# Kernel tuning notes

Hardware: AMD Instinct MI355X
Metric: run time of the kernel (lower is better)

## Reference

```python
import jax, jax.numpy as jnp
import numpy as np

EPS = 1e-7
N = 100000
E = 1600000
IN_DIM = 128
OUT_DIM = 128


def _norm(t):
    # clamped L2 norm over last dim, keepdims
    return jnp.clip(jnp.linalg.norm(t, axis=-1, keepdims=True), EPS, None)


def log_map_zero(x, c):
    sqrt_c = jnp.sqrt(c)
    xn = _norm(x)
    y = jnp.clip(sqrt_c * xn, None, 1.0 - 1e-5)
    return jnp.arctanh(y) * x / (sqrt_c * xn)


def exp_map_zero(v, c):
    sqrt_c = jnp.sqrt(c)
    vn = _norm(v)
    return jnp.tanh(sqrt_c * vn) * v / (sqrt_c * vn)


def setup_inputs() -> dict:
    key = jax.random.key(0)
    k1, k2, k3, k4 = jax.random.split(key, 4)
    x = 0.1 * jax.random.normal(k1, (N, IN_DIM), dtype=jnp.float32)  # inside ball
    edge_index = jax.random.randint(k2, (2, E), 0, N, dtype=jnp.int64)
    c = jnp.ones((), dtype=jnp.float32)
    # Xavier-uniform weight (out_dim, in_dim)
    limit = float(np.sqrt(6.0 / (IN_DIM + OUT_DIM)))
    weight = jax.random.uniform(k3, (OUT_DIM, IN_DIM), minval=-limit, maxval=limit, dtype=jnp.float32)
    bias = jnp.zeros((OUT_DIM,), dtype=jnp.float32)
    return {"x": x, "edge_index": edge_index, "c": c, "num_nodes": N,
            "weight": weight, "bias": bias}


def reference(x, edge_index, c, num_nodes, weight, bias):
    # 1. log-map all node features to tangent space at origin
    v = log_map_zero(x, c)  # (N, in_dim)
    src, dst = edge_index[0], edge_index[1]
    # 2. mean aggregation over neighbours (incl. self) via segment_sum
    agg = jax.ops.segment_sum(v[src], dst, num_segments=num_nodes) + v
    count = jax.ops.segment_sum(jnp.ones((src.shape[0],), dtype=v.dtype), dst,
                                num_segments=num_nodes) + 1.0
    v_agg = agg / jnp.clip(count, 1.0, None)[:, None]
    # 3. back to hyperbolic space, then hyperbolic linear
    x_hyp = exp_map_zero(v_agg, c)
    v2 = log_map_zero(x_hyp, c)
    out = v2 @ weight.T + bias
    return exp_map_zero(out, c)
```

## Files before the change

kernel.cpp:

```cpp
#include <hip/hip_runtime.h>
#include <math.h>

#define EPSF 1e-7f
#define YMAXF 0.99999f
#define WPITCH 136

#define NBUCK 256
#define PB_CHUNK 2048

typedef short bf16x8 __attribute__((ext_vector_type(8)));
typedef short bf16x4 __attribute__((ext_vector_type(4)));
typedef float f32x4  __attribute__((ext_vector_type(4)));

__device__ __forceinline__ float grp32_sum(float v) {
    v += __shfl_xor(v, 1);
    v += __shfl_xor(v, 2);
    v += __shfl_xor(v, 4);
    v += __shfl_xor(v, 8);
    v += __shfl_xor(v, 16);
    return v;
}

__device__ __forceinline__ short f2bf(float f) {
    unsigned u = __float_as_uint(f);
    unsigned r = (u + 0x7FFFu + ((u >> 16) & 1u)) >> 16;
    return (short)r;
}

__device__ __forceinline__ float bf2f(short u) {
    return __uint_as_float(((unsigned)(unsigned short)u) << 16);
}

__global__ void logmap_kernel(const float* __restrict__ x,
                              const float* __restrict__ c_ptr,
                              short* __restrict__ v_bf,
                              int N) {
    int gid = blockIdx.x * blockDim.x + threadIdx.x;
    int row = gid >> 5;
    if (row >= N) return;
    int lane = gid & 31;
    const float4 xv = ((const float4*)x)[(size_t)row * 32 + lane];
    float ss = xv.x * xv.x + xv.y * xv.y + xv.z * xv.z + xv.w * xv.w;
    ss = grp32_sum(ss);
    float sc = sqrtf(c_ptr[0]);
    float xn = fmaxf(sqrtf(ss), EPSF);
    float y = fminf(sc * xn, YMAXF);
    float s = atanhf(y) / (sc * xn);
    bf16x4 pk;
    pk[0] = f2bf(s * xv.x); pk[1] = f2bf(s * xv.y);
    pk[2] = f2bf(s * xv.z); pk[3] = f2bf(s * xv.w);
    *(bf16x4*)&v_bf[(size_t)row * 128 + lane * 4] = pk;
}

__global__ __launch_bounds__(256)
void bucket_count_kernel(const int* __restrict__ eidx_dst,
                         int* __restrict__ bucketCount, int E) {
    __shared__ int h[NBUCK];
    int tid = threadIdx.x;
    h[tid] = 0;
    __syncthreads();
    int per = (E + gridDim.x - 1) / gridDim.x;
    int start = blockIdx.x * per;
    int end = min(start + per, E);
    for (int i = start + tid; i < end; i += 256)
        atomicAdd(&h[eidx_dst[i] >> 9], 1);
    __syncthreads();
    if (h[tid]) atomicAdd(&bucketCount[tid], h[tid]);
}

__global__ __launch_bounds__(256)
void bucket_scan_kernel(const int* __restrict__ bucketCount,
                        int* __restrict__ bucket_base,
                        int* __restrict__ cursor) {
    __shared__ int part[256];
    int tid = threadIdx.x;
    int val = bucketCount[tid];
    part[tid] = val;
    __syncthreads();
    for (int off = 1; off < 256; off <<= 1) {
        int t = (tid >= off) ? part[tid - off] : 0;
        __syncthreads();
        part[tid] += t;
        __syncthreads();
    }
    int excl = part[tid] - val;
    bucket_base[tid] = excl;
    cursor[tid] = excl;
}

__global__ __launch_bounds__(256)
void bucket_scatter_kernel(const int* __restrict__ eidx,
                           int* __restrict__ cursor,
                           int* __restrict__ bucketed, int E) {
    __shared__ int hist[NBUCK];
    __shared__ int lstart[NBUCK];
    __shared__ int gbase[NBUCK];
    __shared__ int part[256];
    __shared__ int stage[PB_CHUNK];
    __shared__ unsigned char stageB[PB_CHUNK];

    int tid = threadIdx.x;
    int start = blockIdx.x * PB_CHUNK;
    int cnt = min(PB_CHUNK, E - start);
    hist[tid] = 0;
    __syncthreads();

    const int J = PB_CHUNK / 256;
    int myP[J], myB[J], myR[J];
    #pragma unroll
    for (int j = 0; j < J; ++j) {
        int idx = j * 256 + tid;
        myR[j] = -1;
        if (idx < cnt) {
            int e = start + idx;
            int d = eidx[E + e];
            int s = eidx[e];
            int b = d >> 9;
            myB[j] = b;
            myP[j] = ((d & 511) << 17) | s;
            myR[j] = atomicAdd(&hist[b], 1);
        }
    }
    __syncthreads();
    part[tid] = hist[tid];
    __syncthreads();
    for (int off = 1; off < 256; off <<= 1) {
        int t = (tid >= off) ? part[tid - off] : 0;
        __syncthreads();
        part[tid] += t;
        __syncthreads();
    }
    lstart[tid] = part[tid] - hist[tid];
    if (hist[tid]) gbase[tid] = atomicAdd(&cursor[tid], hist[tid]);
    __syncthreads();
    #pragma unroll
    for (int j = 0; j < J; ++j) {
        if (myR[j] >= 0) {
            int pos = lstart[myB[j]] + myR[j];
            stage[pos] = myP[j];
            stageB[pos] = (unsigned char)myB[j];
        }
    }
    __syncthreads();
    for (int i = tid; i < cnt; i += 256) {
        int b = stageB[i];
        bucketed[gbase[b] + (i - lstart[b])] = stage[i];
    }
}

__global__ __launch_bounds__(256)
void csr_kernel(const int* __restrict__ bucketed,
                const int* __restrict__ bucket_base,
                const int* __restrict__ cursor_post,
                int* __restrict__ offsets, int* __restrict__ deg,
                int* __restrict__ sorted_src, int N) {
    __shared__ int hist[512];
    __shared__ int pre[512];
    __shared__ int cur[512];
    __shared__ int part[256];
    int b = blockIdx.x;
    int tid = threadIdx.x;
    int start = bucket_base[b];
    int end = cursor_post[b];
    hist[tid] = 0;
    hist[tid + 256] = 0;
    __syncthreads();
    for (int i = start + tid; i < end; i += 256)
        atomicAdd(&hist[bucketed[i] >> 17], 1);
    __syncthreads();
    int a0 = hist[2 * tid], a1 = hist[2 * tid + 1];
    part[tid] = a0 + a1;
    __syncthreads();
    for (int off = 1; off < 256; off <<= 1) {
        int t = (tid >= off) ? part[tid - off] : 0;
        __syncthreads();
        part[tid] += t;
        __syncthreads();
    }
    int base2 = part[tid] - (a0 + a1);
    pre[2 * tid] = base2;
    pre[2 * tid + 1] = base2 + a0;
    cur[2 * tid] = base2;
    cur[2 * tid + 1] = base2 + a0;
    __syncthreads();
    int node0 = b << 9;
    for (int i = tid; i < 512; i += 256) {
        int node = node0 + i;
        if (node < N) { offsets[node] = start + pre[i]; deg[node] = hist[i]; }
    }
    for (int i = start + tid; i < end; i += 256) {
        int p = bucketed[i];
        int ld = p >> 17;
        int src = p & 0x1FFFF;
        int r = atomicAdd(&cur[ld], 1);
        sorted_src[start + r] = src;
    }
}

__global__ __launch_bounds__(256)
void gather_epilogue_kernel(const short* __restrict__ v_bf,
                            const int* __restrict__ sorted_src,
                            const int* __restrict__ offsets,
                            const int* __restrict__ deg,
                            const float* __restrict__ W,
                            const float* __restrict__ bias,
                            const float* __restrict__ c_ptr,
                            float* __restrict__ out,
                            int N, int tiles_per_block) {
    __shared__ short Wl[128 * WPITCH];
    __shared__ short v2l[16 * WPITCH];
    __shared__ float bias_s[128];
    __shared__ float outss[16][4];
    __shared__ float gscale[16];

    int tid = threadIdx.x;
    for (int i = tid; i < 4096; i += 256) {
        float4 w4 = ((const float4*)W)[i];
        int o = i >> 5;
        int k = (i & 31) * 4;
        bf16x4 w;
        w[0] = f2bf(w4.x); w[1] = f2bf(w4.y); w[2] = f2bf(w4.z); w[3] = f2bf(w4.w);
        *(bf16x4*)&Wl[o * WPITCH + k] = w;
    }
    if (tid < 128) bias_s[tid] = bias[tid];
    float sc = sqrtf(c_ptr[0]);
    __syncthreads();

    int wave = tid >> 6;
    int lane = tid & 63;
    int quad = lane >> 4;
    int l16  = lane & 15;
    int g  = tid >> 4;
    int gl = tid & 15;
    int n0 = wave * 32;
    float b0 = bias_s[n0 + l16];
    float b1 = bias_s[n0 + 16 + l16];

    for (int t = 0; t < tiles_per_block; ++t) {
        int row0 = (blockIdx.x * tiles_per_block + t) * 16;
        if (row0 >= N) break;
        int row = row0 + g;
        bool valid = (row < N);

        float acc[8];
        #pragma unroll
        for (int i = 0; i < 8; ++i) acc[i] = 0.0f;
        int start = 0, d = 0;
        if (valid) {
            start = offsets[row];
            d = deg[row];
            bf16x8 r0 = *(const bf16x8*)&v_bf[(size_t)row * 128 + gl * 8];
            #pragma unroll
            for (int i = 0; i < 8; ++i) acc[i] = bf2f(r0[i]);
        }
        for (int j = 0; j < d; j += 16) {
            int idx = j + gl;
            int batch = (idx < d) ? sorted_src[start + idx] : 0;
            int m = min(16, d - j);
            for (int jj = 0; jj < m; ++jj) {
                int src = __shfl(batch, (lane & 48) | jj);
                bf16x8 r = *(const bf16x8*)&v_bf[(size_t)src * 128 + gl * 8];
                #pragma unroll
                for (int i = 0; i < 8; ++i) acc[i] += bf2f(r[i]);
            }
        }
        float inv = 1.0f / (float)(d + 1);
        #pragma unroll
        for (int i = 0; i < 8; ++i) acc[i] *= inv;

        float ss = 0.0f;
        #pragma unroll
        for (int i = 0; i < 8; ++i) ss += acc[i] * acc[i];
        ss += __shfl_xor(ss, 1);
        ss += __shfl_xor(ss, 2);
        ss += __shfl_xor(ss, 4);
        ss += __shfl_xor(ss, 8);

        float vn  = sqrtf(ss);
        float vnc = fmaxf(vn, EPSF);
        float th  = tanhf(sc * vnc);
        float tt  = th / (sc * vnc);
        float hn  = fmaxf(th / sc, EPSF);
        float y2  = fminf(sc * hn, YMAXF);
        float s2  = atanhf(y2) / (sc * hn);
        float scale = s2 * tt;

        bf16x8 pk;
        #pragma unroll
        for (int i = 0; i < 8; ++i) pk[i] = f2bf(acc[i] * scale);
        *(bf16x8*)&v2l[g * WPITCH + gl * 8] = pk;
        __syncthreads();

        f32x4 acc0 = {b0, b0, b0, b0};
        f32x4 acc1 = {b1, b1, b1, b1};
        #pragma unroll
        for (int k0 = 0; k0 < 128; k0 += 32) {
            bf16x8 af  = *(const bf16x8*)&v2l[l16 * WPITCH + k0 + quad * 8];
            bf16x8 bf0 = *(const bf16x8*)&Wl[(n0 + l16) * WPITCH + k0 + quad * 8];
            bf16x8 bf1 = *(const bf16x8*)&Wl[(n0 + 16 + l16) * WPITCH + k0 + quad * 8];
            acc0 = __builtin_amdgcn_mfma_f32_16x16x32_bf16(af, bf0, acc0, 0, 0, 0);
            acc1 = __builtin_amdgcn_mfma_f32_16x16x32_bf16(af, bf1, acc1, 0, 0, 0);
        }

        float pss[4];
        #pragma unroll
        for (int r = 0; r < 4; ++r) {
            float vsum = acc0[r]*acc0[r] + acc1[r]*acc1[r];
            vsum += __shfl_xor(vsum, 1);
            vsum += __shfl_xor(vsum, 2);
            vsum += __shfl_xor(vsum, 4);
            vsum += __shfl_xor(vsum, 8);
            pss[r] = vsum;
        }
        if (l16 == 0) {
            #pragma unroll
            for (int r = 0; r < 4; ++r) outss[quad * 4 + r][wave] = pss[r];
        }
        __syncthreads();
        if (tid < 16) {
            float on  = sqrtf(outss[tid][0] + outss[tid][1] + outss[tid][2] + outss[tid][3]);
            float onc = fmaxf(on, EPSF);
            gscale[tid] = tanhf(sc * onc) / (sc * onc);
        }
        __syncthreads();
        #pragma unroll
        for (int r = 0; r < 4; ++r) {
            int orow = quad * 4 + r;
            if (row0 + orow < N) {
                float gsc = gscale[orow];
                size_t base = (size_t)(row0 + orow) * 128;
                out[base + n0 + l16]      = gsc * acc0[r];
                out[base + n0 + 16 + l16] = gsc * acc1[r];
            }
        }
        __syncthreads();
    }
}

extern "C" void kernel_launch(void* const* d_in, const int* in_sizes, int n_in,
                              void* d_out, int out_size, void* d_ws, size_t ws_size,
                              hipStream_t stream) {
    const float* x     = (const float*)d_in[0];
    const int*   eidx  = (const int*)d_in[1];
    const float* c_ptr = (const float*)d_in[2];
    const float* W     = (const float*)d_in[4];
    const float* bias  = (const float*)d_in[5];
    float* out = (float*)d_out;

    int N = in_sizes[0] / 128;
    int E = in_sizes[1] / 2;

    short* v_bf        = (short*)d_ws;
    int*   deg         = (int*)(v_bf + (size_t)N * 128);
    int*   offsets     = deg + N;
    int*   bucketCount = offsets + N;
    int*   bucket_base = bucketCount + NBUCK;
    int*   cursor      = bucket_base + NBUCK;
    int*   bucketed    = cursor + NBUCK;
    int*   sorted_src  = bucketed + E;

    hipMemsetAsync(bucketCount, 0, NBUCK * sizeof(int), stream);

    {
        long long threads = (long long)N * 32;
        int blocks = (int)((threads + 255) / 256);
        hipLaunchKernelGGL(logmap_kernel, dim3(blocks), dim3(256), 0, stream,
                           x, c_ptr, v_bf, N);
    }
    hipLaunchKernelGGL(bucket_count_kernel, dim3(256), dim3(256), 0, stream,
                       eidx + E, bucketCount, E);
    hipLaunchKernelGGL(bucket_scan_kernel, dim3(1), dim3(256), 0, stream,
                       bucketCount, bucket_base, cursor);
    {
        int blocks = (E + PB_CHUNK - 1) / PB_CHUNK;
        hipLaunchKernelGGL(bucket_scatter_kernel, dim3(blocks), dim3(256), 0, stream,
                           eidx, cursor, bucketed, E);
    }
    {
        int blocks = (N + 511) / 512;
        hipLaunchKernelGGL(csr_kernel, dim3(blocks), dim3(256), 0, stream,
                           bucketed, bucket_base, cursor, offsets, deg, sorted_src, N);
    }
    {
        const int TPB = 5;
        int numTiles = (N + 15) / 16;
        int blocks = (numTiles + TPB - 1) / TPB;
        hipLaunchKernelGGL(gather_epilogue_kernel, dim3(blocks), dim3(256), 0, stream,
                           v_bf, sorted_src, offsets, deg, W, bias, c_ptr, out, N, TPB);
    }
}
```

Before: 312.2 us.

## Batch neighbor loads and restructure gather epilogue into 64-row blocks with per-wave GEMM

```diff
diff --git a/kernel.cpp b/kernel.cpp
--- a/kernel.cpp
+++ b/kernel.cpp
@@ -11,6 +11,7 @@
 typedef short bf16x8 __attribute__((ext_vector_type(8)));
 typedef short bf16x4 __attribute__((ext_vector_type(4)));
 typedef float f32x4  __attribute__((ext_vector_type(4)));
+typedef int   i32x4  __attribute__((ext_vector_type(4)));
 
 __device__ __forceinline__ float grp32_sum(float v) {
     v += __shfl_xor(v, 1);
@@ -29,6 +30,13 @@
 
 __device__ __forceinline__ float bf2f(short u) {
     return __uint_as_float(((unsigned)(unsigned short)u) << 16);
+}
+
+__device__ __forceinline__ float bf_lo(int w) {
+    return __uint_as_float(((unsigned)w) << 16);
+}
+__device__ __forceinline__ float bf_hi(int w) {
+    return __uint_as_float(((unsigned)w) & 0xffff0000u);
 }
 
 __global__ void logmap_kernel(const float* __restrict__ x,
@@ -197,7 +205,7 @@
     }
 }
 
-__global__ __launch_bounds__(256)
+__global__ __launch_bounds__(256, 3)
 void gather_epilogue_kernel(const short* __restrict__ v_bf,
                             const int* __restrict__ sorted_src,
                             const int* __restrict__ offsets,
@@ -206,12 +214,9 @@
                             const float* __restrict__ bias,
                             const float* __restrict__ c_ptr,
                             float* __restrict__ out,
-                            int N, int tiles_per_block) {
+                            int N) {
     __shared__ short Wl[128 * WPITCH];
-    __shared__ short v2l[16 * WPITCH];
-    __shared__ float bias_s[128];
-    __shared__ float outss[16][4];
-    __shared__ float gscale[16];
+    __shared__ short v2l[64 * WPITCH];
 
     int tid = threadIdx.x;
     for (int i = tid; i < 4096; i += 256) {
@@ -222,9 +227,6 @@
         w[0] = f2bf(w4.x); w[1] = f2bf(w4.y); w[2] = f2bf(w4.z); w[3] = f2bf(w4.w);
         *(bf16x4*)&Wl[o * WPITCH + k] = w;
     }
-    if (tid < 128) bias_s[tid] = bias[tid];
-    float sc = sqrtf(c_ptr[0]);
-    __syncthreads();
 
     int wave = tid >> 6;
     int lane = tid & 63;
@@ -232,16 +234,17 @@
     int l16  = lane & 15;
     int g  = tid >> 4;
     int gl = tid & 15;
-    int n0 = wave * 32;
-    float b0 = bias_s[n0 + l16];
-    float b1 = bias_s[n0 + 16 + l16];
-
-    for (int t = 0; t < tiles_per_block; ++t) {
-        int row0 = (blockIdx.x * tiles_per_block + t) * 16;
-        if (row0 >= N) break;
-        int row = row0 + g;
+    float sc = sqrtf(c_ptr[0]);
+
+    float bsv[8];
+    #pragma unroll
+    for (int c = 0; c < 8; ++c) bsv[c] = bias[c * 16 + l16];
+
+    int row_base = blockIdx.x * 64;
+
+    for (int t = 0; t < 4; ++t) {
+        int row = row_base + t * 16 + g;
         bool valid = (row < N);
-
         float acc[8];
         #pragma unroll
         for (int i = 0; i < 8; ++i) acc[i] = 0.0f;
@@ -250,18 +253,35 @@
             start = offsets[row];
             d = deg[row];
             bf16x8 r0 = *(const bf16x8*)&v_bf[(size_t)row * 128 + gl * 8];
+            i32x4 w0 = *(const i32x4*)&r0;
             #pragma unroll
-            for (int i = 0; i < 8; ++i) acc[i] = bf2f(r0[i]);
+            for (int k2 = 0; k2 < 4; ++k2) {
+                acc[2 * k2]     = bf_lo(w0[k2]);
+                acc[2 * k2 + 1] = bf_hi(w0[k2]);
+            }
         }
         for (int j = 0; j < d; j += 16) {
+            int m = d - j;
             int idx = j + gl;
-            int batch = (idx < d) ? sorted_src[start + idx] : 0;
-            int m = min(16, d - j);
-            for (int jj = 0; jj < m; ++jj) {
-                int src = __shfl(batch, (lane & 48) | jj);
-                bf16x8 r = *(const bf16x8*)&v_bf[(size_t)src * 128 + gl * 8];
-                #pragma unroll
-                for (int i = 0; i < 8; ++i) acc[i] += bf2f(r[i]);
+            int batch = sorted_src[start + min(idx, d - 1)];
+            bf16x8 r[16];
+            #pragma unroll
+            for (int jj = 0; jj < 16; ++jj) {
+                if (jj < m) {
+                    int src = __shfl(batch, (lane & 48) | jj);
+                    r[jj] = *(const bf16x8*)&v_bf[(size_t)src * 128 + gl * 8];
+                }
+            }
+            #pragma unroll
+            for (int jj = 0; jj < 16; ++jj) {
+                if (jj < m) {
+                    i32x4 wv = *(const i32x4*)&r[jj];
+                    #pragma unroll
+                    for (int k2 = 0; k2 < 4; ++k2) {
+                        acc[2 * k2]     += bf_lo(wv[k2]);
+                        acc[2 * k2 + 1] += bf_hi(wv[k2]);
+                    }
+                }
             }
         }
         float inv = 1.0f / (float)(d + 1);
@@ -288,52 +308,42 @@
         bf16x8 pk;
         #pragma unroll
         for (int i = 0; i < 8; ++i) pk[i] = f2bf(acc[i] * scale);
-        *(bf16x8*)&v2l[g * WPITCH + gl * 8] = pk;
-        __syncthreads();
-
-        f32x4 acc0 = {b0, b0, b0, b0};
-        f32x4 acc1 = {b1, b1, b1, b1};
-        #pragma unroll
-        for (int k0 = 0; k0 < 128; k0 += 32) {
-            bf16x8 af  = *(const bf16x8*)&v2l[l16 * WPITCH + k0 + quad * 8];
-            bf16x8 bf0 = *(const bf16x8*)&Wl[(n0 + l16) * WPITCH + k0 + quad * 8];
-            bf16x8 bf1 = *(const bf16x8*)&Wl[(n0 + 16 + l16) * WPITCH + k0 + quad * 8];
-            acc0 = __builtin_amdgcn_mfma_f32_16x16x32_bf16(af, bf0, acc0, 0, 0, 0);
-            acc1 = __builtin_amdgcn_mfma_f32_16x16x32_bf16(af, bf1, acc1, 0, 0, 0);
-        }
-
-        float pss[4];
-        #pragma unroll
-        for (int r = 0; r < 4; ++r) {
-            float vsum = acc0[r]*acc0[r] + acc1[r]*acc1[r];
-            vsum += __shfl_xor(vsum, 1);
-            vsum += __shfl_xor(vsum, 2);
-            vsum += __shfl_xor(vsum, 4);
-            vsum += __shfl_xor(vsum, 8);
-            pss[r] = vsum;
-        }
-        if (l16 == 0) {
+        *(bf16x8*)&v2l[(t * 16 + g) * WPITCH + gl * 8] = pk;
+    }
+    __syncthreads();
+
+    f32x4 acc2[8];
+    #pragma unroll
+    for (int c = 0; c < 8; ++c) acc2[c] = (f32x4){bsv[c], bsv[c], bsv[c], bsv[c]};
+    #pragma unroll
+    for (int k0 = 0; k0 < 128; k0 += 32) {
+        bf16x8 af = *(const bf16x8*)&v2l[(wave * 16 + l16) * WPITCH + k0 + quad * 8];
+        #pragma unroll
+        for (int c = 0; c < 8; ++c) {
+            bf16x8 bf = *(const bf16x8*)&Wl[(c * 16 + l16) * WPITCH + k0 + quad * 8];
+            acc2[c] = __builtin_amdgcn_mfma_f32_16x16x32_bf16(af, bf, acc2[c], 0, 0, 0);
+        }
+    }
+
+    #pragma unroll
+    for (int r = 0; r < 4; ++r) {
+        float ss = 0.0f;
+        #pragma unroll
+        for (int c = 0; c < 8; ++c) ss += acc2[c][r] * acc2[c][r];
+        ss += __shfl_xor(ss, 1);
+        ss += __shfl_xor(ss, 2);
+        ss += __shfl_xor(ss, 4);
+        ss += __shfl_xor(ss, 8);
+        float on  = sqrtf(ss);
+        float onc = fmaxf(on, EPSF);
+        float gsc = tanhf(sc * onc) / (sc * onc);
+        int orow = row_base + wave * 16 + quad * 4 + r;
+        if (orow < N) {
+            size_t base = (size_t)orow * 128;
             #pragma unroll
-            for (int r = 0; r < 4; ++r) outss[quad * 4 + r][wave] = pss[r];
-        }
-        __syncthreads();
-        if (tid < 16) {
-            float on  = sqrtf(outss[tid][0] + outss[tid][1] + outss[tid][2] + outss[tid][3]);
-            float onc = fmaxf(on, EPSF);
-            gscale[tid] = tanhf(sc * onc) / (sc * onc);
-        }
-        __syncthreads();
-        #pragma unroll
-        for (int r = 0; r < 4; ++r) {
-            int orow = quad * 4 + r;
-            if (row0 + orow < N) {
-                float gsc = gscale[orow];
-                size_t base = (size_t)(row0 + orow) * 128;
-                out[base + n0 + l16]      = gsc * acc0[r];
-                out[base + n0 + 16 + l16] = gsc * acc1[r];
-            }
-        }
-        __syncthreads();
+            for (int c = 0; c < 8; ++c)
+                out[base + c * 16 + l16] = gsc * acc2[c][r];
+        }
     }
 }
 
@@ -382,10 +392,8 @@
                            bucketed, bucket_base, cursor, offsets, deg, sorted_src, N);
     }
     {
-        const int TPB = 5;
-        int numTiles = (N + 15) / 16;
-        int blocks = (numTiles + TPB - 1) / TPB;
+        int blocks = (N + 63) / 64;
         hipLaunchKernelGGL(gather_epilogue_kernel, dim3(blocks), dim3(256), 0, stream,
-                           v_bf, sorted_src, offsets, deg, W, bias, c_ptr, out, N, TPB);
-    }
-}
+                           v_bf, sorted_src, offsets, deg, W, bias, c_ptr, out, N);
+    }
+}
```

After: 316.6 us. Within noise of the previous version (+1.4%).
